# Kernel tuning notes

Measured on AMD Instinct MI355X. Metric: run time of the kernel, lower is better.

The kernel has to match this reference:

```python
import jax, jax.numpy as jnp
import numpy as np

# dims
N = 10000      # nodes
E = 320000     # edges (avg degree 32)
NS = 64        # hidden 0e scalar channels
NV = 64        # hidden 1o vector channels
EMB = 32       # node-attr embedding dim
NTYPES = 20    # max_atom_types
NB = 8         # number_of_basis (bessel)
RH = 16        # radial_neurons
L = 2          # layers
CUT = 3.5      # max_radius
NNEIGH = 32.0  # num_neighbors normalization
H = 0.1        # residual step size


def smooth_cutoff(u):
    # e3nn example smooth_cutoff applied to x/max_radius
    v = 2.0 * (u - 1.0)
    y = 0.5 * (1.0 - jnp.cos(jnp.pi * v))
    y = jnp.where(v > 0.0, 0.0, y)
    y = jnp.where(v < -1.0, 1.0, y)
    return y


def setup_inputs() -> dict:
    key = jax.random.key(0)
    ks = jax.random.split(key, 10)
    x = jax.random.normal(ks[0], (N, 6), jnp.float32)
    batch = jnp.zeros((N,), jnp.int32)
    node_attr = jax.random.randint(ks[1], (N,), 0, NTYPES)
    edge_src = jax.random.randint(ks[2], (E,), 0, N)
    # avoid self-loops (zero edge length -> NaN in sh / bessel)
    off = jax.random.randint(ks[3], (E,), 1, N)
    edge_dst = (edge_src + off) % N
    embed_table = 0.1 * jax.random.normal(ks[4], (NTYPES, EMB), jnp.float32)
    Ku = jax.random.normal(ks[5], (2, NV), jnp.float32)          # uplift (made semi-unitary via QR)
    W_sc_s = 0.05 * jax.random.normal(ks[6], (L, NS, EMB, NS + NV), jnp.float32)  # self-connection TP: scalars
    W_sc_v = 0.05 * jax.random.normal(ks[7], (L, NV, EMB, NV), jnp.float32)       # self-connection TP: vectors
    Wr1 = 0.3 * jax.random.normal(ks[8], (L, NB, RH), jnp.float32)
    br1 = jnp.zeros((L, RH), jnp.float32)
    Wr2 = 0.3 * jax.random.normal(ks[9], (L, RH, 4 * NV), jnp.float32)
    br2 = jnp.zeros((L, 4 * NV), jnp.float32)
    return {"x": x, "batch": batch, "node_attr": node_attr, "edge_src": edge_src,
            "edge_dst": edge_dst, "embed_table": embed_table, "Ku": Ku,
            "W_sc_s": W_sc_s, "W_sc_v": W_sc_v, "Wr1": Wr1, "br1": br1,
            "Wr2": Wr2, "br2": br2}


def reference(x, batch, node_attr, edge_src, edge_dst, embed_table, Ku,
              W_sc_s, W_sc_v, Wr1, br1, Wr2, br2):
    n = x.shape[0]
    a = embed_table[node_attr]                     # [n, EMB] node-attr embedding (0e scalars)
    # make uplift semi-unitary: Q^T Q = I_2
    Q, _ = jnp.linalg.qr(Ku.T)                     # [NV, 2]
    U = Q.T                                        # uplift [2, NV]
    x_v = x.reshape(n, 2, 3)                       # 2x1o: position, velocity
    y_s = jnp.zeros((n, NS), x.dtype)              # uplift has no 1o->0e path
    y_v = jnp.einsum('ncd,ch->nhd', x_v, U)        # [n, NV, 3]
    nfreq = jnp.arange(1, NB + 1, dtype=x.dtype)
    inv_deg = 1.0 / np.sqrt(NNEIGH)
    for l in range(L):
        pos = x_v[:, 0, :]
        ev = pos[edge_src] - pos[edge_dst]                          # [E, 3]
        elen = jnp.linalg.norm(ev, axis=1)                          # [E]
        sh = jnp.sqrt(3.0) * ev / elen[:, None]                     # 1x1o SH, component norm
        # bessel radial basis, scaled by sqrt(NB)
        bess = (jnp.sqrt(2.0 / CUT) * jnp.sin(jnp.pi * nfreq * elen[:, None] / CUT)
                / elen[:, None]) * np.sqrt(NB)                      # [E, NB]
        ea = smooth_cutoff(elen / CUT)[:, None] * sh                # edge_attr [E, 3]
        # radial MLP -> per-edge tensor-product weights (4 paths x NV channels)
        w = jax.nn.silu(bess @ Wr1[l] + br1[l]) @ Wr2[l] + br2[l]   # [E, 4*NV]
        wA, wB, wC, wD = jnp.split(w, 4, axis=1)
        s_src = y_s[edge_src]                                       # [E, NS]
        v_src = y_v[edge_src]                                       # [E, NV, 3]
        # TP paths: 0e x 1o -> 1o ; 1o x 1o -> 1o (cross) ; 1o x 1o -> 0e (dot, feats + gates)
        msg_v = (wA[:, :, None] * s_src[:, :, None] * ea[:, None, :]
                 + wC[:, :, None] * jnp.cross(v_src, ea[:, None, :]))  # [E, NV, 3]
        dots = jnp.einsum('evd,ed->ev', v_src, ea)                  # [E, NV]
        msg_s = jnp.concatenate([wB * dots, wD * dots], axis=1)     # [E, NS+NV]
        agg_s = jax.ops.segment_sum(msg_s, edge_dst, num_segments=n) * inv_deg
        agg_v = (jax.ops.segment_sum(msg_v.reshape(msg_v.shape[0], -1), edge_dst,
                                     num_segments=n).reshape(n, NV, 3) * inv_deg)
        # self-connection: fully-connected TP with node-attr scalars
        sc_s = jnp.einsum('ns,ne,seo->no', y_s, a, W_sc_s[l])       # [n, NS+NV]
        sc_v = jnp.einsum('nvd,ne,veu->nud', y_v, a, W_sc_v[l])     # [n, NV, 3]
        out_s = sc_s + agg_s
        out_v = sc_v + agg_v
        # gate: silu on scalar feats, sigmoid gates scale the vectors
        y_s = y_s + H * jax.nn.silu(out_s[:, :NS])
        y_v = y_v + H * jax.nn.sigmoid(out_s[:, NS:])[:, :, None] * out_v
        # project back to 2x1o
        x_v = jnp.einsum('nhd,hc->ncd', y_v, Q)
    return x_v.reshape(n, 6)
```

## Files before the change

### kernel.cpp

```cpp
#include <hip/hip_runtime.h>
#include <math.h>

#define NSC 64
#define NVC 64
#define EMB 32
#define NTYPES 20
#define NB 8
#define RH 16
#define LAYERS 2
#define CUTV 3.5f
#define HSTEP 0.1f

__device__ __forceinline__ float wave_sum(float t)
{
  #pragma unroll
  for (int mm = 1; mm < 64; mm <<= 1) t += __shfl_xor(t, mm, 64);
  return t;
}

__global__ void qr_kernel(const float* __restrict__ Ku, float* __restrict__ Q)
{
  const int i = threadIdx.x;
  float a0 = Ku[i], a1 = Ku[64 + i];
  const float xn2 = wave_sum((i >= 1) ? a0 * a0 : 0.f);
  const float alpha = __shfl(a0, 0, 64);
  const float beta0 = -copysignf(sqrtf(alpha * alpha + xn2), alpha);
  const float tau0 = (beta0 - alpha) / beta0;
  const float inv0 = 1.f / (alpha - beta0);
  const float v0 = (i == 0) ? 1.f : a0 * inv0;
  const float w = wave_sum(v0 * a1);
  a1 -= tau0 * w * v0;
  const float alpha1 = __shfl(a1, 1, 64);
  const float xn2b = wave_sum((i >= 2) ? a1 * a1 : 0.f);
  const float beta1 = -copysignf(sqrtf(alpha1 * alpha1 + xn2b), alpha1);
  const float tau1 = (beta1 - alpha1) / beta1;
  const float inv1 = 1.f / (alpha1 - beta1);
  const float v1 = (i == 0) ? 0.f : ((i == 1) ? 1.f : a1 * inv1);
  const float t1v = ((i == 1) ? 1.f : 0.f) - tau1 * v1;
  const float d = wave_sum(v0 * t1v);
  Q[i * 2 + 0] = ((i == 0) ? 1.f : 0.f) - tau0 * v0;
  Q[i * 2 + 1] = t1v - tau0 * d * v0;
}

__global__ void init_state(const float* __restrict__ x, const float* __restrict__ Qm,
                           float4* __restrict__ st0, int* __restrict__ cnt, int n)
{
  const int i = blockIdx.x * 256 + threadIdx.x;
  const int node = i >> 6, lane = i & 63;
  if (node < n) {
    const float q0 = Qm[lane * 2 + 0], q1 = Qm[lane * 2 + 1];
    const float* xp = x + (size_t)node * 6;
    st0[i] = make_float4(0.f,
                         xp[0] * q0 + xp[3] * q1,
                         xp[1] * q0 + xp[4] * q1,
                         xp[2] * q0 + xp[5] * q1);
  }
  if (i < n) cnt[i] = 0;
}

__global__ void hist_kernel(const int* __restrict__ edst, int* __restrict__ cnt, int m)
{
  const int e = blockIdx.x * 256 + threadIdx.x;
  if (e < m) atomicAdd(&cnt[edst[e]], 1);
}

__global__ void scan_kernel(int* cnt, int* off, int n)
{
  __shared__ int lds[1024];
  const int t = threadIdx.x;
  const int CH = (n + 1023) >> 10;
  const int base = t * CH;
  int local[16];
  int run = 0;
  for (int j = 0; j < CH; ++j) {
    int v = (base + j < n) ? cnt[base + j] : 0;
    local[j] = run;
    run += v;
  }
  lds[t] = run;
  __syncthreads();
  for (int s = 1; s < 1024; s <<= 1) {
    int v = (t >= s) ? lds[t - s] : 0;
    __syncthreads();
    lds[t] += v;
    __syncthreads();
  }
  const int excl = lds[t] - run;
  for (int j = 0; j < CH; ++j) {
    if (base + j < n) {
      int o = excl + local[j];
      off[base + j] = o;
      cnt[base + j] = o;
    }
  }
  if (t == 1023) off[n] = lds[1023];
}

__global__ void scatter_kernel(const int* __restrict__ edst, int* __restrict__ cursor,
                               int* __restrict__ csr, int m)
{
  const int e = blockIdx.x * 256 + threadIdx.x;
  if (e < m) {
    int p = atomicAdd(&cursor[edst[e]], 1);
    csr[p] = e;
  }
}

__global__ void reorder_kernel(const int* __restrict__ csr,
                               const int* __restrict__ esrc, const int* __restrict__ edst,
                               int* __restrict__ esrc_s, int* __restrict__ edst_s, int m)
{
  const int k = blockIdx.x * 256 + threadIdx.x;
  if (k < m) {
    const int e = csr[k];
    esrc_s[k] = esrc[e];
    edst_s[k] = edst[e];
  }
}

__global__ void type_weights(const float* __restrict__ embed,
                             const float* __restrict__ Wss,
                             const float* __restrict__ Wsv,
                             float* __restrict__ Ws, float* __restrict__ Wv,
                             int total_s, int total_v)
{
  const int i = blockIdx.x * 256 + threadIdx.x;
  if (i < total_s) {
    const int bid = i >> 13;
    const int p = i & 8191;
    const int l = bid / NTYPES, t = bid % NTYPES;
    const int s = p >> 7, o = p & 127;
    const float* ar = embed + t * EMB;
    const float* wp = Wss + ((size_t)(l * 64 + s) * EMB) * 128 + o;
    float acc = 0.f;
    #pragma unroll
    for (int e = 0; e < EMB; ++e) acc = fmaf(ar[e], wp[e * 128], acc);
    Ws[i] = acc;
  } else {
    const int j = i - total_s;
    if (j < total_v) {
      const int bid = j >> 12;
      const int p = j & 4095;
      const int l = bid / NTYPES, t = bid % NTYPES;
      const int v = p >> 6, u = p & 63;
      const float* ar = embed + t * EMB;
      const float* wp = Wsv + ((size_t)(l * 64 + v) * EMB) * 64 + u;
      float acc = 0.f;
      #pragma unroll
      for (int e = 0; e < EMB; ++e) acc = fmaf(ar[e], wp[e * 64], acc);
      Wv[j] = acc;
    }
  }
}

__global__ void transpose_wr2(const float* __restrict__ Wr2, float* __restrict__ Wt)
{
  const int t = blockIdx.x * 256 + threadIdx.x;
  if (t >= LAYERS * 256) return;
  const int l = t >> 8, ch = t & 255;
  #pragma unroll
  for (int j = 0; j < RH; ++j)
    Wt[(size_t)l * 4096 + ch * RH + j] = Wr2[(size_t)l * 4096 + j * 256 + ch];
}

__global__ void edge_geom(const float* __restrict__ xv,
                          const int* __restrict__ esrc_s, const int* __restrict__ edst_s,
                          const float* __restrict__ Wr1l, const float* __restrict__ br1l,
                          float4* __restrict__ ea4, float* __restrict__ hidb, int m)
{
  const int k = blockIdx.x * 256 + threadIdx.x;
  if (k >= m) return;
  const int s = esrc_s[k], d = edst_s[k];
  const float ex = xv[(size_t)s * 6 + 0] - xv[(size_t)d * 6 + 0];
  const float ey = xv[(size_t)s * 6 + 1] - xv[(size_t)d * 6 + 1];
  const float ez = xv[(size_t)s * 6 + 2] - xv[(size_t)d * 6 + 2];
  const float len = sqrtf(ex * ex + ey * ey + ez * ez);
  const float invl = 1.f / len;
  const float u = len * (1.f / CUTV);
  const float arg = (float)M_PI * u;
  float sa, ca;
  __sincosf(arg, &sa, &ca);
  const float vv = 2.f * (u - 1.f);
  float cut = 0.5f * (1.f - (2.f * ca * ca - 1.f));
  cut = (vv > 0.f) ? 0.f : cut;
  cut = (vv < -1.f) ? 1.f : cut;
  const float cc = cut * 1.7320508075688772f * invl;
  ea4[k] = make_float4(cc * ex, cc * ey, cc * ez, 0.f);
  float bess[NB];
  const float amp = 2.1380899352993948f * invl;
  const float twoc = 2.f * ca;
  float sm1 = 0.f, scur = sa;
  #pragma unroll
  for (int kk = 0; kk < NB; ++kk) {
    bess[kk] = amp * scur;
    const float snext = twoc * scur - sm1;
    sm1 = scur; scur = snext;
  }
  float hid[RH];
  #pragma unroll
  for (int j = 0; j < RH; ++j) {
    float h = br1l[j];
    #pragma unroll
    for (int kk = 0; kk < NB; ++kk) h = fmaf(bess[kk], Wr1l[kk * RH + j], h);
    hid[j] = h / (1.f + expf(-h));
  }
  float4* hp = (float4*)(hidb + (size_t)k * 16);
  hp[0] = make_float4(hid[0],  hid[1],  hid[2],  hid[3]);
  hp[1] = make_float4(hid[4],  hid[5],  hid[6],  hid[7]);
  hp[2] = make_float4(hid[8],  hid[9],  hid[10], hid[11]);
  hp[3] = make_float4(hid[12], hid[13], hid[14], hid[15]);
}

#define PIN_LOAD4(dst, addr)                                                  \
  asm volatile("global_load_dwordx4 %0, %1, off" : "=v"(dst) : "v"(addr) : "memory")

#define MLP16(res, W0, W1, W2, W3)                                            \
  res = fmaf(g1.x, W0.x, res); res = fmaf(g1.y, W0.y, res);                   \
  res = fmaf(g1.z, W0.z, res); res = fmaf(g1.w, W0.w, res);                   \
  res = fmaf(g2.x, W1.x, res); res = fmaf(g2.y, W1.y, res);                   \
  res = fmaf(g2.z, W1.z, res); res = fmaf(g2.w, W1.w, res);                   \
  res = fmaf(g3.x, W2.x, res); res = fmaf(g3.y, W2.y, res);                   \
  res = fmaf(g3.z, W2.z, res); res = fmaf(g3.w, W2.w, res);                   \
  res = fmaf(g4.x, W3.x, res); res = fmaf(g4.y, W3.y, res);                   \
  res = fmaf(g4.z, W3.z, res); res = fmaf(g4.w, W3.w, res);

__global__ __launch_bounds__(256, 2) void gather_update(
    const int* __restrict__ off, const int* __restrict__ esrc_s,
    const float4* __restrict__ ea4, const float* __restrict__ hidb,
    const float4* __restrict__ st_in, const int* __restrict__ nattr,
    const float* __restrict__ Ws, const float* __restrict__ Wv,
    const float* __restrict__ Wtl, const float* __restrict__ br2l,
    const float* __restrict__ Qm,
    float4* __restrict__ st_out, float* __restrict__ xv_out, int n)
{
  const int lane = threadIdx.x & 63;
  const int node = blockIdx.x * 4 + (threadIdx.x >> 6);
  if (node >= n) return;

  float4 WA0, WA1, WA2, WA3, WB0, WB1, WB2, WB3;
  float4 WC0, WC1, WC2, WC3, WD0, WD1, WD2, WD3;
  {
    const float* pa = Wtl + (size_t)lane * RH;
    const float* pb = Wtl + (size_t)(64 + lane) * RH;
    const float* pc = Wtl + (size_t)(128 + lane) * RH;
    const float* pd = Wtl + (size_t)(192 + lane) * RH;
    PIN_LOAD4(WA0, pa);  PIN_LOAD4(WA1, pa + 4);  PIN_LOAD4(WA2, pa + 8);  PIN_LOAD4(WA3, pa + 12);
    PIN_LOAD4(WB0, pb);  PIN_LOAD4(WB1, pb + 4);  PIN_LOAD4(WB2, pb + 8);  PIN_LOAD4(WB3, pb + 12);
    PIN_LOAD4(WC0, pc);  PIN_LOAD4(WC1, pc + 4);  PIN_LOAD4(WC2, pc + 8);  PIN_LOAD4(WC3, pc + 12);
    PIN_LOAD4(WD0, pd);  PIN_LOAD4(WD1, pd + 4);  PIN_LOAD4(WD2, pd + 8);  PIN_LOAD4(WD3, pd + 12);
    asm volatile("s_waitcnt vmcnt(0)" ::: "memory");
    __builtin_amdgcn_sched_barrier(0);
  }
  const float bA = br2l[lane], bB = br2l[64 + lane],
              bC = br2l[128 + lane], bD = br2l[192 + lane];

  float aS1 = 0.f, aS2 = 0.f, aV0 = 0.f, aV1 = 0.f, aV2 = 0.f;
  const int k0 = off[node], k1 = off[node + 1];
  if (k0 < k1) {
    int srcN = esrc_s[k0];
    float4 stN = st_in[(size_t)srcN * 64 + lane];
    float4 eaN = ea4[k0];
    const float4* hN = (const float4*)(hidb + (size_t)k0 * 16);
    float4 g1N = hN[0], g2N = hN[1], g3N = hN[2], g4N = hN[3];
    srcN = (k0 + 1 < k1) ? esrc_s[k0 + 1] : srcN;

    for (int k = k0; k < k1; ++k) {
      const float4 stc = stN, ea = eaN;
      const float4 g1 = g1N, g2 = g2N, g3 = g3N, g4 = g4N;
      stN = st_in[(size_t)srcN * 64 + lane];
      const int kn = (k + 1 < k1) ? (k + 1) : k;
      eaN = ea4[kn];
      const float4* hp = (const float4*)(hidb + (size_t)kn * 16);
      g1N = hp[0]; g2N = hp[1]; g3N = hp[2]; g4N = hp[3];
      srcN = (k + 2 < k1) ? esrc_s[k + 2] : srcN;
      float wA = bA, wB = bB, wC = bC, wD = bD;
      MLP16(wA, WA0, WA1, WA2, WA3)
      MLP16(wB, WB0, WB1, WB2, WB3)
      MLP16(wC, WC0, WC1, WC2, WC3)
      MLP16(wD, WD0, WD1, WD2, WD3)
      const float ss = stc.x, vx = stc.y, vy = stc.z, vz = stc.w;
      const float dt = vx * ea.x + vy * ea.y + vz * ea.z;
      aS1 = fmaf(wB, dt, aS1);
      aS2 = fmaf(wD, dt, aS2);
      const float t = wA * ss;
      aV0 += t * ea.x + wC * (vy * ea.z - vz * ea.y);
      aV1 += t * ea.y + wC * (vz * ea.x - vx * ea.z);
      aV2 += t * ea.z + wC * (vx * ea.y - vy * ea.x);
    }
  }
  const float inv_deg = 0.17677669529663687f;

  const int ty = nattr[node];
  const float* WsT = Ws + (size_t)ty * 8192;
  const float* WvT = Wv + (size_t)ty * 4096;
  const float4 own = st_in[(size_t)node * 64 + lane];
  const float ys_own = own.x, v0x = own.y, v0y = own.z, v0z = own.w;
  float oS1 = 0.f, oS2 = 0.f, oV0 = 0.f, oV1 = 0.f, oV2 = 0.f;
  #pragma unroll 4
  for (int s2 = 0; s2 < 64; ++s2) {
    const float yss = __shfl(ys_own, s2, 64);
    const float b0 = __shfl(v0x, s2, 64);
    const float b1 = __shfl(v0y, s2, 64);
    const float b2 = __shfl(v0z, s2, 64);
    const float wsA = WsT[s2 * 128 + lane];
    const float wsB = WsT[s2 * 128 + 64 + lane];
    const float wvv = WvT[s2 * 64 + lane];
    oS1 = fmaf(yss, wsA, oS1);
    oS2 = fmaf(yss, wsB, oS2);
    oV0 = fmaf(b0, wvv, oV0);
    oV1 = fmaf(b1, wvv, oV1);
    oV2 = fmaf(b2, wvv, oV2);
  }
  const float outS1 = oS1 + aS1 * inv_deg;
  const float outS2 = oS2 + aS2 * inv_deg;
  const float sig1 = 1.f / (1.f + expf(-outS1));
  const float gate = 1.f / (1.f + expf(-outS2));
  const float ysn = ys_own + HSTEP * outS1 * sig1;
  const float gf = HSTEP * gate;
  const float yvn0 = v0x + gf * (oV0 + aV0 * inv_deg);
  const float yvn1 = v0y + gf * (oV1 + aV1 * inv_deg);
  const float yvn2 = v0z + gf * (oV2 + aV2 * inv_deg);
  st_out[(size_t)node * 64 + lane] = make_float4(ysn, yvn0, yvn1, yvn2);

  const float q0 = Qm[lane * 2 + 0], q1 = Qm[lane * 2 + 1];
  float pr[6] = { yvn0 * q0, yvn1 * q0, yvn2 * q0,
                  yvn0 * q1, yvn1 * q1, yvn2 * q1 };
  #pragma unroll
  for (int mm = 1; mm < 64; mm <<= 1) {
    #pragma unroll
    for (int i = 0; i < 6; ++i) pr[i] += __shfl_xor(pr[i], mm, 64);
  }
  if (lane == 0) {
    #pragma unroll
    for (int i = 0; i < 6; ++i) xv_out[(size_t)node * 6 + i] = pr[i];
  }
}

extern "C" void kernel_launch(void* const* d_in, const int* in_sizes, int n_in,
                              void* d_out, int out_size, void* d_ws, size_t ws_size,
                              hipStream_t stream)
{
  const float* x     = (const float*)d_in[0];
  const int*   nattr = (const int*)d_in[2];
  const int*   esrc  = (const int*)d_in[3];
  const int*   edst  = (const int*)d_in[4];
  const float* embed = (const float*)d_in[5];
  const float* Ku    = (const float*)d_in[6];
  const float* Wss   = (const float*)d_in[7];
  const float* Wsv   = (const float*)d_in[8];
  const float* Wr1   = (const float*)d_in[9];
  const float* br1   = (const float*)d_in[10];
  const float* Wr2   = (const float*)d_in[11];
  const float* br2   = (const float*)d_in[12];
  const int n = in_sizes[0] / 6;
  const int m = in_sizes[3];

  char* p = (char*)d_ws;
  auto alloc = [&](size_t bytes) -> char* {
    char* r = p;
    p += (bytes + 255) & ~(size_t)255;
    return r;
  };
  int*    off    = (int*)alloc((size_t)(n + 1) * 4);
  int*    cursor = (int*)alloc((size_t)n * 4);
  int*    csr    = (int*)alloc((size_t)m * 4);
  int*    esrc_s = (int*)alloc((size_t)m * 4);
  int*    edst_s = (int*)alloc((size_t)m * 4);
  float*  Q      = (float*)alloc(128 * 4);
  float*  Ws     = (float*)alloc((size_t)LAYERS * NTYPES * 64 * 128 * 4);
  float*  Wv     = (float*)alloc((size_t)LAYERS * NTYPES * 64 * 64 * 4);
  float4* st0    = (float4*)alloc((size_t)n * 64 * 16);
  float4* st1    = (float4*)alloc((size_t)n * 64 * 16);
  float*  xvb    = (float*)alloc((size_t)n * 6 * 4);
  float4* ea4    = (float4*)alloc((size_t)m * 16);
  float*  hidb   = (float*)alloc((size_t)m * 16 * 4);
  float*  Wt     = (float*)alloc((size_t)LAYERS * 4096 * 4);

  const int total_s = LAYERS * NTYPES * 64 * 128;
  const int total_v = LAYERS * NTYPES * 64 * 64;

  qr_kernel<<<1, 64, 0, stream>>>(Ku, Q);
  init_state<<<(n * 64 + 255) / 256, 256, 0, stream>>>(x, Q, st0, cursor, n);
  hist_kernel<<<(m + 255) / 256, 256, 0, stream>>>(edst, cursor, m);
  scan_kernel<<<1, 1024, 0, stream>>>(cursor, off, n);
  scatter_kernel<<<(m + 255) / 256, 256, 0, stream>>>(edst, cursor, csr, m);
  reorder_kernel<<<(m + 255) / 256, 256, 0, stream>>>(csr, esrc, edst, esrc_s, edst_s, m);
  type_weights<<<(total_s + total_v + 255) / 256, 256, 0, stream>>>(
      embed, Wss, Wsv, Ws, Wv, total_s, total_v);
  transpose_wr2<<<2, 256, 0, stream>>>(Wr2, Wt);

  const float* xv_cur = x;
  const float4* st_cur = st0;
  float4* st_nxt = st1;
  for (int l = 0; l < LAYERS; ++l) {
    edge_geom<<<(m + 255) / 256, 256, 0, stream>>>(
        xv_cur, esrc_s, edst_s, Wr1 + l * NB * RH, br1 + l * RH, ea4, hidb, m);
    float* xv_out = (l == LAYERS - 1) ? (float*)d_out : xvb;
    gather_update<<<(n + 3) / 4, 256, 0, stream>>>(
        off, esrc_s, ea4, hidb, st_cur, nattr,
        Ws + (size_t)l * NTYPES * 8192, Wv + (size_t)l * NTYPES * 4096,
        Wt + (size_t)l * 4096, br2 + l * 256, Q,
        st_nxt, xv_out, n);
    xv_cur = xv_out;
    float4* ts = (float4*)st_cur; st_cur = st_nxt; st_nxt = ts;
  }
}
```

Measured before the change: 321.6 us.

## Split per-node gather across four waves by radial weight group

Measured after the change: 343.6 us. 1.07x slower.

```diff
diff --git a/kernel.cpp b/kernel.cpp
--- a/kernel.cpp
+++ b/kernel.cpp
@@ -211,20 +211,37 @@
   hp[3] = make_float4(hid[12], hid[13], hid[14], hid[15]);
 }
 
-#define PIN_LOAD4(dst, addr)                                                  \
-  asm volatile("global_load_dwordx4 %0, %1, off" : "=v"(dst) : "v"(addr) : "memory")
-
-#define MLP16(res, W0, W1, W2, W3)                                            \
-  res = fmaf(g1.x, W0.x, res); res = fmaf(g1.y, W0.y, res);                   \
-  res = fmaf(g1.z, W0.z, res); res = fmaf(g1.w, W0.w, res);                   \
-  res = fmaf(g2.x, W1.x, res); res = fmaf(g2.y, W1.y, res);                   \
-  res = fmaf(g2.z, W1.z, res); res = fmaf(g2.w, W1.w, res);                   \
-  res = fmaf(g3.x, W2.x, res); res = fmaf(g3.y, W2.y, res);                   \
-  res = fmaf(g3.z, W2.z, res); res = fmaf(g3.w, W2.w, res);                   \
-  res = fmaf(g4.x, W3.x, res); res = fmaf(g4.y, W3.y, res);                   \
-  res = fmaf(g4.z, W3.z, res); res = fmaf(g4.w, W3.w, res);
-
-__global__ __launch_bounds__(256, 2) void gather_update(
+#define EDGE_PIPELINE(QSTMT)                                                  \
+  {                                                                           \
+    int srcN = esrc_s[k0];                                                    \
+    float4 stN = st_in[(size_t)srcN * 64 + lane];                             \
+    const float4* hp0 = (const float4*)(hidb + (size_t)k0 * 16);              \
+    float4 h0N = hp0[0], h1N = hp0[1], h2N = hp0[2], h3N = hp0[3];            \
+    float4 eaN = ea4[k0];                                                     \
+    srcN = (k0 + 1 < k1) ? esrc_s[k0 + 1] : srcN;                             \
+    for (int k = k0; k < k1; ++k) {                                           \
+      const float4 stc = stN, ea = eaN;                                       \
+      const float4 g1 = h0N, g2 = h1N, g3 = h2N, g4 = h3N;                    \
+      stN = st_in[(size_t)srcN * 64 + lane];                                  \
+      const int kn = (k + 1 < k1) ? (k + 1) : k;                              \
+      const float4* hp = (const float4*)(hidb + (size_t)kn * 16);             \
+      h0N = hp[0]; h1N = hp[1]; h2N = hp[2]; h3N = hp[3];                     \
+      eaN = ea4[kn];                                                          \
+      srcN = (k + 2 < k1) ? esrc_s[k + 2] : srcN;                             \
+      float w = bias;                                                         \
+      w = fmaf(g1.x, W0.x, w); w = fmaf(g1.y, W0.y, w);                       \
+      w = fmaf(g1.z, W0.z, w); w = fmaf(g1.w, W0.w, w);                       \
+      w = fmaf(g2.x, W1.x, w); w = fmaf(g2.y, W1.y, w);                       \
+      w = fmaf(g2.z, W1.z, w); w = fmaf(g2.w, W1.w, w);                       \
+      w = fmaf(g3.x, W2.x, w); w = fmaf(g3.y, W2.y, w);                       \
+      w = fmaf(g3.z, W2.z, w); w = fmaf(g3.w, W2.w, w);                       \
+      w = fmaf(g4.x, W3.x, w); w = fmaf(g4.y, W3.y, w);                       \
+      w = fmaf(g4.z, W3.z, w); w = fmaf(g4.w, W3.w, w);                       \
+      QSTMT                                                                   \
+    }                                                                         \
+  }
+
+__global__ __launch_bounds__(256, 4) void gather_update(
     const int* __restrict__ off, const int* __restrict__ esrc_s,
     const float4* __restrict__ ea4, const float* __restrict__ hidb,
     const float4* __restrict__ st_in, const int* __restrict__ nattr,
@@ -233,106 +250,110 @@
     const float* __restrict__ Qm,
     float4* __restrict__ st_out, float* __restrict__ xv_out, int n)
 {
+  __shared__ float eAx[64], eAy[64], eAz[64], eCx[64], eCy[64], eCz[64];
+  __shared__ float eB[64], eD[64];
+  __shared__ float oP[4][5][64];
   const int lane = threadIdx.x & 63;
-  const int node = blockIdx.x * 4 + (threadIdx.x >> 6);
-  if (node >= n) return;
-
-  float4 WA0, WA1, WA2, WA3, WB0, WB1, WB2, WB3;
-  float4 WC0, WC1, WC2, WC3, WD0, WD1, WD2, WD3;
-  {
-    const float* pa = Wtl + (size_t)lane * RH;
-    const float* pb = Wtl + (size_t)(64 + lane) * RH;
-    const float* pc = Wtl + (size_t)(128 + lane) * RH;
-    const float* pd = Wtl + (size_t)(192 + lane) * RH;
-    PIN_LOAD4(WA0, pa);  PIN_LOAD4(WA1, pa + 4);  PIN_LOAD4(WA2, pa + 8);  PIN_LOAD4(WA3, pa + 12);
-    PIN_LOAD4(WB0, pb);  PIN_LOAD4(WB1, pb + 4);  PIN_LOAD4(WB2, pb + 8);  PIN_LOAD4(WB3, pb + 12);
-    PIN_LOAD4(WC0, pc);  PIN_LOAD4(WC1, pc + 4);  PIN_LOAD4(WC2, pc + 8);  PIN_LOAD4(WC3, pc + 12);
-    PIN_LOAD4(WD0, pd);  PIN_LOAD4(WD1, pd + 4);  PIN_LOAD4(WD2, pd + 8);  PIN_LOAD4(WD3, pd + 12);
-    asm volatile("s_waitcnt vmcnt(0)" ::: "memory");
-    __builtin_amdgcn_sched_barrier(0);
-  }
-  const float bA = br2l[lane], bB = br2l[64 + lane],
-              bC = br2l[128 + lane], bD = br2l[192 + lane];
-
-  float aS1 = 0.f, aS2 = 0.f, aV0 = 0.f, aV1 = 0.f, aV2 = 0.f;
+  const int wid = threadIdx.x >> 6;
+  const int node = blockIdx.x;
+
+  const int chg = (wid << 6) + lane;
+  const float* wp = Wtl + (size_t)chg * RH;
+  const float4 W0 = *(const float4*)wp;
+  const float4 W1 = *(const float4*)(wp + 4);
+  const float4 W2 = *(const float4*)(wp + 8);
+  const float4 W3 = *(const float4*)(wp + 12);
+  const float bias = br2l[chg];
+
+  float a0 = 0.f, a1 = 0.f, a2 = 0.f;
   const int k0 = off[node], k1 = off[node + 1];
   if (k0 < k1) {
-    int srcN = esrc_s[k0];
-    float4 stN = st_in[(size_t)srcN * 64 + lane];
-    float4 eaN = ea4[k0];
-    const float4* hN = (const float4*)(hidb + (size_t)k0 * 16);
-    float4 g1N = hN[0], g2N = hN[1], g3N = hN[2], g4N = hN[3];
-    srcN = (k0 + 1 < k1) ? esrc_s[k0 + 1] : srcN;
-
-    for (int k = k0; k < k1; ++k) {
-      const float4 stc = stN, ea = eaN;
-      const float4 g1 = g1N, g2 = g2N, g3 = g3N, g4 = g4N;
-      stN = st_in[(size_t)srcN * 64 + lane];
-      const int kn = (k + 1 < k1) ? (k + 1) : k;
-      eaN = ea4[kn];
-      const float4* hp = (const float4*)(hidb + (size_t)kn * 16);
-      g1N = hp[0]; g2N = hp[1]; g3N = hp[2]; g4N = hp[3];
-      srcN = (k + 2 < k1) ? esrc_s[k + 2] : srcN;
-      float wA = bA, wB = bB, wC = bC, wD = bD;
-      MLP16(wA, WA0, WA1, WA2, WA3)
-      MLP16(wB, WB0, WB1, WB2, WB3)
-      MLP16(wC, WC0, WC1, WC2, WC3)
-      MLP16(wD, WD0, WD1, WD2, WD3)
-      const float ss = stc.x, vx = stc.y, vy = stc.z, vz = stc.w;
-      const float dt = vx * ea.x + vy * ea.y + vz * ea.z;
-      aS1 = fmaf(wB, dt, aS1);
-      aS2 = fmaf(wD, dt, aS2);
-      const float t = wA * ss;
-      aV0 += t * ea.x + wC * (vy * ea.z - vz * ea.y);
-      aV1 += t * ea.y + wC * (vz * ea.x - vx * ea.z);
-      aV2 += t * ea.z + wC * (vx * ea.y - vy * ea.x);
-    }
-  }
-  const float inv_deg = 0.17677669529663687f;
+    if (wid == 0) {
+      EDGE_PIPELINE({
+        const float t = w * stc.x;
+        a0 = fmaf(t, ea.x, a0); a1 = fmaf(t, ea.y, a1); a2 = fmaf(t, ea.z, a2);
+      })
+    } else if (wid == 1) {
+      EDGE_PIPELINE({
+        const float dt = stc.y * ea.x + stc.z * ea.y + stc.w * ea.z;
+        a0 = fmaf(w, dt, a0);
+      })
+    } else if (wid == 2) {
+      EDGE_PIPELINE({
+        a0 = fmaf(w, stc.z * ea.z - stc.w * ea.y, a0);
+        a1 = fmaf(w, stc.w * ea.x - stc.y * ea.z, a1);
+        a2 = fmaf(w, stc.y * ea.y - stc.z * ea.x, a2);
+      })
+    } else {
+      EDGE_PIPELINE({
+        const float dt = stc.y * ea.x + stc.z * ea.y + stc.w * ea.z;
+        a0 = fmaf(w, dt, a0);
+      })
+    }
+  }
+  if (wid == 0)      { eAx[lane] = a0; eAy[lane] = a1; eAz[lane] = a2; }
+  else if (wid == 1) { eB[lane] = a0; }
+  else if (wid == 2) { eCx[lane] = a0; eCy[lane] = a1; eCz[lane] = a2; }
+  else               { eD[lane] = a0; }
 
   const int ty = nattr[node];
   const float* WsT = Ws + (size_t)ty * 8192;
   const float* WvT = Wv + (size_t)ty * 4096;
   const float4 own = st_in[(size_t)node * 64 + lane];
-  const float ys_own = own.x, v0x = own.y, v0y = own.z, v0z = own.w;
   float oS1 = 0.f, oS2 = 0.f, oV0 = 0.f, oV1 = 0.f, oV2 = 0.f;
+  const int s20 = wid << 4;
   #pragma unroll 4
-  for (int s2 = 0; s2 < 64; ++s2) {
-    const float yss = __shfl(ys_own, s2, 64);
-    const float b0 = __shfl(v0x, s2, 64);
-    const float b1 = __shfl(v0y, s2, 64);
-    const float b2 = __shfl(v0z, s2, 64);
-    const float wsA = WsT[s2 * 128 + lane];
-    const float wsB = WsT[s2 * 128 + 64 + lane];
+  for (int s2 = s20; s2 < s20 + 16; ++s2) {
+    const float yss = __shfl(own.x, s2, 64);
+    const float b0 = __shfl(own.y, s2, 64);
+    const float b1 = __shfl(own.z, s2, 64);
+    const float b2 = __shfl(own.w, s2, 64);
+    oS1 = fmaf(yss, WsT[s2 * 128 + lane], oS1);
+    oS2 = fmaf(yss, WsT[s2 * 128 + 64 + lane], oS2);
     const float wvv = WvT[s2 * 64 + lane];
-    oS1 = fmaf(yss, wsA, oS1);
-    oS2 = fmaf(yss, wsB, oS2);
     oV0 = fmaf(b0, wvv, oV0);
     oV1 = fmaf(b1, wvv, oV1);
     oV2 = fmaf(b2, wvv, oV2);
   }
-  const float outS1 = oS1 + aS1 * inv_deg;
-  const float outS2 = oS2 + aS2 * inv_deg;
-  const float sig1 = 1.f / (1.f + expf(-outS1));
-  const float gate = 1.f / (1.f + expf(-outS2));
-  const float ysn = ys_own + HSTEP * outS1 * sig1;
-  const float gf = HSTEP * gate;
-  const float yvn0 = v0x + gf * (oV0 + aV0 * inv_deg);
-  const float yvn1 = v0y + gf * (oV1 + aV1 * inv_deg);
-  const float yvn2 = v0z + gf * (oV2 + aV2 * inv_deg);
-  st_out[(size_t)node * 64 + lane] = make_float4(ysn, yvn0, yvn1, yvn2);
-
-  const float q0 = Qm[lane * 2 + 0], q1 = Qm[lane * 2 + 1];
-  float pr[6] = { yvn0 * q0, yvn1 * q0, yvn2 * q0,
-                  yvn0 * q1, yvn1 * q1, yvn2 * q1 };
-  #pragma unroll
-  for (int mm = 1; mm < 64; mm <<= 1) {
+  oP[wid][0][lane] = oS1; oP[wid][1][lane] = oS2;
+  oP[wid][2][lane] = oV0; oP[wid][3][lane] = oV1; oP[wid][4][lane] = oV2;
+  __syncthreads();
+
+  if (wid == 0) {
+    const float inv_deg = 0.17677669529663687f;
+    const float aS1 = eB[lane], aS2 = eD[lane];
+    const float aV0 = eAx[lane] + eCx[lane];
+    const float aV1 = eAy[lane] + eCy[lane];
+    const float aV2 = eAz[lane] + eCz[lane];
+    float s1 = 0.f, s2v = 0.f, v0 = 0.f, v1 = 0.f, v2 = 0.f;
     #pragma unroll
-    for (int i = 0; i < 6; ++i) pr[i] += __shfl_xor(pr[i], mm, 64);
-  }
-  if (lane == 0) {
+    for (int q = 0; q < 4; ++q) {
+      s1 += oP[q][0][lane]; s2v += oP[q][1][lane];
+      v0 += oP[q][2][lane]; v1 += oP[q][3][lane]; v2 += oP[q][4][lane];
+    }
+    const float outS1 = s1 + aS1 * inv_deg;
+    const float outS2 = s2v + aS2 * inv_deg;
+    const float sig1 = 1.f / (1.f + expf(-outS1));
+    const float gate = 1.f / (1.f + expf(-outS2));
+    const float ysn = own.x + HSTEP * outS1 * sig1;
+    const float gf = HSTEP * gate;
+    const float yvn0 = own.y + gf * (v0 + aV0 * inv_deg);
+    const float yvn1 = own.z + gf * (v1 + aV1 * inv_deg);
+    const float yvn2 = own.w + gf * (v2 + aV2 * inv_deg);
+    st_out[(size_t)node * 64 + lane] = make_float4(ysn, yvn0, yvn1, yvn2);
+
+    const float q0 = Qm[lane * 2 + 0], q1 = Qm[lane * 2 + 1];
+    float pr[6] = { yvn0 * q0, yvn1 * q0, yvn2 * q0,
+                    yvn0 * q1, yvn1 * q1, yvn2 * q1 };
     #pragma unroll
-    for (int i = 0; i < 6; ++i) xv_out[(size_t)node * 6 + i] = pr[i];
+    for (int mm = 1; mm < 64; mm <<= 1) {
+      #pragma unroll
+      for (int i = 0; i < 6; ++i) pr[i] += __shfl_xor(pr[i], mm, 64);
+    }
+    if (lane == 0) {
+      #pragma unroll
+      for (int i = 0; i < 6; ++i) xv_out[(size_t)node * 6 + i] = pr[i];
+    }
   }
 }
 
@@ -396,7 +417,7 @@
     edge_geom<<<(m + 255) / 256, 256, 0, stream>>>(
         xv_cur, esrc_s, edst_s, Wr1 + l * NB * RH, br1 + l * RH, ea4, hidb, m);
     float* xv_out = (l == LAYERS - 1) ? (float*)d_out : xvb;
-    gather_update<<<(n + 3) / 4, 256, 0, stream>>>(
+    gather_update<<<n, 256, 0, stream>>>(
         off, esrc_s, ea4, hidb, st_cur, nattr,
         Ws + (size_t)l * NTYPES * 8192, Wv + (size_t)l * NTYPES * 4096,
         Wt + (size_t)l * 4096, br2 + l * 256, Q,
```
